# Kernel tuning notes

Hardware: AMD Instinct MI355X
Metric: run time of the kernel (lower is better)

## Reference

```python
import jax, jax.numpy as jnp
import numpy as np
import math

D_MODEL = 1024
N_HEADS = 16
HEAD_DIM = D_MODEL // N_HEADS
N, S = 8, 4096


def setup_inputs() -> dict:
    key = jax.random.key(0)
    ks = jax.random.split(key, 11)
    s = 1.0 / math.sqrt(D_MODEL)
    return {
        "Q": jax.random.normal(ks[0], (N, 1, D_MODEL), jnp.float32),
        "K": jax.random.normal(ks[1], (N, S, D_MODEL), jnp.float32),
        "V": jax.random.normal(ks[2], (N, S, D_MODEL), jnp.float32),
        "Wq": jax.random.normal(ks[3], (D_MODEL, D_MODEL), jnp.float32) * s,
        "bq": jax.random.normal(ks[4], (D_MODEL,), jnp.float32) * s,
        "Wk": jax.random.normal(ks[5], (D_MODEL, D_MODEL), jnp.float32) * s,
        "bk": jax.random.normal(ks[6], (D_MODEL,), jnp.float32) * s,
        "Wv": jax.random.normal(ks[7], (D_MODEL, D_MODEL), jnp.float32) * s,
        "bv": jax.random.normal(ks[8], (D_MODEL,), jnp.float32) * s,
        "Wo": jax.random.normal(ks[9], (D_MODEL, D_MODEL), jnp.float32) * s,
        "bo": jax.random.normal(ks[10], (D_MODEL,), jnp.float32) * s,
    }


def reference(Q, K, V, Wq, bq, Wk, bk, Wv, bv, Wo, bo):
    n, s_len, d = K.shape
    h, hd = N_HEADS, HEAD_DIM
    # Linear projections (torch Linear: y = x @ W.T + b)
    q = (Q @ Wq.T + bq).reshape(n, 1, h, hd)        # [n,1,h,hd]
    k = (K @ Wk.T + bk).reshape(n, s_len, h, hd)    # [n,s,h,hd]
    v = (V @ Wv.T + bv).reshape(n, s_len, h, hd)
    # scores: einsum('npqk,nqsk->nqsp') with K transposed to [n,h,s,hd]
    scores = jnp.einsum('npqk,nqsk->nqsp', q, k.transpose(0, 2, 1, 3)) / math.sqrt(hd)  # [n,h,s,1]
    # NOTE: faithful to source: softmax over the LAST dim, which has size 1 -> all-ones weights
    attn = jax.nn.softmax(scores, axis=-1)  # [n,h,s,1]
    wv = jnp.einsum('nqsp,nqsk->nqpk', attn, v.transpose(0, 2, 1, 3))  # [n,h,1,hd]
    # combine heads: transpose(-2,-3) -> [n,1,h,hd], then flatten to [n,1,d]
    concat = wv.transpose(0, 2, 1, 3).reshape(-1, 1, d)
    return concat @ Wo.T + bo
```

## Files before the change

### kernel.cpp

```cpp
#include <hip/hip_runtime.h>

#define D_MODEL 1024
#define NB      8
#define SLEN    4096
#define D4      (D_MODEL / 4)
#define GROUPS  64
#define ROWS_PER_GROUP (SLEN / GROUPS)
#define NBLOCKS (NB * GROUPS)

__global__ __launch_bounds__(256) void vsum_partial_kernel(
    const float* __restrict__ V, float4* __restrict__ partials) {
    const int b = blockIdx.x;
    const int t = threadIdx.x;
    const int n = b >> 6;
    const int g = b & 63;

    const float4* Vb = (const float4*)(V + (size_t)n * SLEN * D_MODEL);
    const size_t base = (size_t)g * ROWS_PER_GROUP * D4 + t;

    float4 acc = make_float4(0.f, 0.f, 0.f, 0.f);
#pragma unroll 8
    for (int r = 0; r < ROWS_PER_GROUP; ++r) {
        float4 x = Vb[base + (size_t)r * D4];
        acc.x += x.x; acc.y += x.y; acc.z += x.z; acc.w += x.w;
    }
    partials[(size_t)b * D4 + t] = acc;
}

__global__ __launch_bounds__(256) void vsum_reduce_kernel(
    const float4* __restrict__ partials, float4* __restrict__ Vsum) {
    const int n = blockIdx.x;
    const int t = threadIdx.x;
    float4 acc = make_float4(0.f, 0.f, 0.f, 0.f);
#pragma unroll 8
    for (int g = 0; g < GROUPS; ++g) {
        float4 x = partials[((size_t)n * GROUPS + g) * D4 + t];
        acc.x += x.x; acc.y += x.y; acc.z += x.z; acc.w += x.w;
    }
    Vsum[(size_t)n * D4 + t] = acc;
}

__global__ __launch_bounds__(256) void gemv8_kernel(
    const float4* __restrict__ X,
    const float*  __restrict__ W,
    const float*  __restrict__ bvec,
    float* __restrict__ Y,
    float bias_scale) {
    const int t    = threadIdx.x;
    const int wv   = t >> 6;
    const int lane = t & 63;
    const int i    = blockIdx.x * 4 + wv;

    const float4* Wr = (const float4*)(W + (size_t)i * D_MODEL);

    float acc[NB];
#pragma unroll
    for (int n = 0; n < NB; ++n) acc[n] = 0.f;

#pragma unroll
    for (int g = lane; g < D4; g += 64) {
        float4 w = Wr[g];
#pragma unroll
        for (int n = 0; n < NB; ++n) {
            float4 x = X[n * D4 + g];
            acc[n] += w.x * x.x + w.y * x.y + w.z * x.z + w.w * x.w;
        }
    }

#pragma unroll
    for (int n = 0; n < NB; ++n) {
        float v = acc[n];
#pragma unroll
        for (int off = 32; off > 0; off >>= 1) v += __shfl_down(v, off);
        if (lane == 0) Y[(size_t)n * D_MODEL + i] = v + bias_scale * bvec[i];
    }
}

extern "C" void kernel_launch(void* const* d_in, const int* in_sizes, int n_in,
                              void* d_out, int out_size, void* d_ws, size_t ws_size,
                              hipStream_t stream) {
    const float* V  = (const float*)d_in[2];
    const float* Wv = (const float*)d_in[7];
    const float* bv = (const float*)d_in[8];
    const float* Wo = (const float*)d_in[9];
    const float* bo = (const float*)d_in[10];
    float* out = (float*)d_out;

    float4* partials = (float4*)d_ws;
    float4* Vsum     = partials + (size_t)NBLOCKS * D4;
    float4* vproj    = Vsum + NB * D4;

    vsum_partial_kernel<<<NBLOCKS, 256, 0, stream>>>(V, partials);
    vsum_reduce_kernel<<<NB, 256, 0, stream>>>(partials, Vsum);
    gemv8_kernel<<<D_MODEL / 4, 256, 0, stream>>>(Vsum, Wv, bv, (float*)vproj,
                                                  (float)SLEN);
    gemv8_kernel<<<D_MODEL / 4, 256, 0, stream>>>(vproj, Wo, bo, out, 1.0f);
}
```

Measured before the change: 275.9 us.

## Fuse V-sum, reduction and two GEMVs into one cooperative kernel

Replaces four kernel launches with one cooperative-groups kernel that uses grid.sync between the partial V column sum, the per-batch reduction, and the two GEMV stages. The partial-sum stage now uses 128 groups, which gives 1024 blocks so that each block handles one output column in each GEMV, with a shared-memory cross-wave reduction. The aim is to remove launch gaps and tail effects between the small stages. In exchange it adds grid-wide barriers, and it needs all 1024 blocks to be co-resident for the cooperative launch.

```diff
diff --git a/kernel.cpp b/kernel.cpp
--- a/kernel.cpp
+++ b/kernel.cpp
@@ -1,79 +1,92 @@
 #include <hip/hip_runtime.h>
+#include <hip/hip_cooperative_groups.h>
+
+namespace cg = cooperative_groups;
 
 #define D_MODEL 1024
 #define NB      8
 #define SLEN    4096
 #define D4      (D_MODEL / 4)
-#define GROUPS  64
+#define GROUPS  128
 #define ROWS_PER_GROUP (SLEN / GROUPS)
 #define NBLOCKS (NB * GROUPS)
 
-__global__ __launch_bounds__(256) void vsum_partial_kernel(
-    const float* __restrict__ V, float4* __restrict__ partials) {
-    const int b = blockIdx.x;
-    const int t = threadIdx.x;
-    const int n = b >> 6;
-    const int g = b & 63;
-
-    const float4* Vb = (const float4*)(V + (size_t)n * SLEN * D_MODEL);
-    const size_t base = (size_t)g * ROWS_PER_GROUP * D4 + t;
-
-    float4 acc = make_float4(0.f, 0.f, 0.f, 0.f);
-#pragma unroll 8
-    for (int r = 0; r < ROWS_PER_GROUP; ++r) {
-        float4 x = Vb[base + (size_t)r * D4];
-        acc.x += x.x; acc.y += x.y; acc.z += x.z; acc.w += x.w;
-    }
-    partials[(size_t)b * D4 + t] = acc;
-}
-
-__global__ __launch_bounds__(256) void vsum_reduce_kernel(
-    const float4* __restrict__ partials, float4* __restrict__ Vsum) {
-    const int n = blockIdx.x;
-    const int t = threadIdx.x;
-    float4 acc = make_float4(0.f, 0.f, 0.f, 0.f);
-#pragma unroll 8
-    for (int g = 0; g < GROUPS; ++g) {
-        float4 x = partials[((size_t)n * GROUPS + g) * D4 + t];
-        acc.x += x.x; acc.y += x.y; acc.z += x.z; acc.w += x.w;
-    }
-    Vsum[(size_t)n * D4 + t] = acc;
-}
-
-__global__ __launch_bounds__(256) void gemv8_kernel(
+__device__ __forceinline__ void gemv_col(
     const float4* __restrict__ X,
     const float*  __restrict__ W,
     const float*  __restrict__ bvec,
     float* __restrict__ Y,
-    float bias_scale) {
-    const int t    = threadIdx.x;
-    const int wv   = t >> 6;
-    const int lane = t & 63;
-    const int i    = blockIdx.x * 4 + wv;
-
-    const float4* Wr = (const float4*)(W + (size_t)i * D_MODEL);
-
+    float bias_scale, int i, int t, float (*red)[NB])
+{
+    const float4 w = ((const float4*)(W + (size_t)i * D_MODEL))[t];
     float acc[NB];
 #pragma unroll
-    for (int n = 0; n < NB; ++n) acc[n] = 0.f;
-
-#pragma unroll
-    for (int g = lane; g < D4; g += 64) {
-        float4 w = Wr[g];
-#pragma unroll
-        for (int n = 0; n < NB; ++n) {
-            float4 x = X[n * D4 + g];
-            acc[n] += w.x * x.x + w.y * x.y + w.z * x.z + w.w * x.w;
-        }
+    for (int n = 0; n < NB; ++n) {
+        float4 x = X[n * D4 + t];
+        acc[n] = w.x * x.x + w.y * x.y + w.z * x.z + w.w * x.w;
     }
-
+    const int lane = t & 63;
+    const int wv   = t >> 6;
 #pragma unroll
     for (int n = 0; n < NB; ++n) {
-        float v = acc[n];
 #pragma unroll
-        for (int off = 32; off > 0; off >>= 1) v += __shfl_down(v, off);
-        if (lane == 0) Y[(size_t)n * D_MODEL + i] = v + bias_scale * bvec[i];
+        for (int off = 32; off > 0; off >>= 1)
+            acc[n] += __shfl_down(acc[n], off);
     }
+    if (lane == 0) {
+#pragma unroll
+        for (int n = 0; n < NB; ++n) red[wv][n] = acc[n];
+    }
+    __syncthreads();
+    if (t < NB)
+        Y[(size_t)t * D_MODEL + i] =
+            red[0][t] + red[1][t] + red[2][t] + red[3][t] + bias_scale * bvec[i];
+}
+
+__global__ __launch_bounds__(256, 4) void fused_kernel(
+    const float* __restrict__ V,
+    const float* __restrict__ Wv, const float* __restrict__ bv,
+    const float* __restrict__ Wo, const float* __restrict__ bo,
+    float* __restrict__ out,
+    float4* __restrict__ partials,
+    float4* __restrict__ Vsum,
+    float4* __restrict__ vproj)
+{
+    cg::grid_group grid = cg::this_grid();
+    const int b = blockIdx.x;
+    const int t = threadIdx.x;
+    __shared__ float red[4][NB];
+
+    {
+        const int n = b >> 7;
+        const int g = b & (GROUPS - 1);
+        const float4* Vb = (const float4*)(V + (size_t)n * SLEN * D_MODEL);
+        const size_t base = (size_t)g * ROWS_PER_GROUP * D4 + t;
+        float4 acc = make_float4(0.f, 0.f, 0.f, 0.f);
+#pragma unroll 8
+        for (int r = 0; r < ROWS_PER_GROUP; ++r) {
+            float4 x = Vb[base + (size_t)r * D4];
+            acc.x += x.x; acc.y += x.y; acc.z += x.z; acc.w += x.w;
+        }
+        partials[(size_t)b * D4 + t] = acc;
+    }
+    grid.sync();
+
+    if (b < NB) {
+        float4 acc = make_float4(0.f, 0.f, 0.f, 0.f);
+#pragma unroll 8
+        for (int g = 0; g < GROUPS; ++g) {
+            float4 x = partials[((size_t)b * GROUPS + g) * D4 + t];
+            acc.x += x.x; acc.y += x.y; acc.z += x.z; acc.w += x.w;
+        }
+        Vsum[b * D4 + t] = acc;
+    }
+    grid.sync();
+
+    gemv_col(Vsum, Wv, bv, (float*)vproj, (float)SLEN, b, t, red);
+    grid.sync();
+
+    gemv_col(vproj, Wo, bo, out, 1.0f, b, t, red);
 }
 
 extern "C" void kernel_launch(void* const* d_in, const int* in_sizes, int n_in,
@@ -90,9 +103,8 @@
     float4* Vsum     = partials + (size_t)NBLOCKS * D4;
     float4* vproj    = Vsum + NB * D4;
 
-    vsum_partial_kernel<<<NBLOCKS, 256, 0, stream>>>(V, partials);
-    vsum_reduce_kernel<<<NB, 256, 0, stream>>>(partials, Vsum);
-    gemv8_kernel<<<D_MODEL / 4, 256, 0, stream>>>(Vsum, Wv, bv, (float*)vproj,
-                                                  (float)SLEN);
-    gemv8_kernel<<<D_MODEL / 4, 256, 0, stream>>>(vproj, Wo, bo, out, 1.0f);
+    void* args[] = {(void*)&V,  (void*)&Wv, (void*)&bv, (void*)&Wo, (void*)&bo,
+                    (void*)&out, (void*)&partials, (void*)&Vsum, (void*)&vproj};
+    hipLaunchCooperativeKernel((const void*)fused_kernel, dim3(NBLOCKS),
+                               dim3(256), args, 0, stream);
 }
```

Measured after the change: 618.0 us. 2.24x slower.
